# Performance work log

Measured on AMD Instinct MI355X. Metric: run time of the kernel, lower is better.

Reference implementation:

```python
import jax, jax.numpy as jnp
import numpy as np

N = 100_000
E = 1_000_000
F_IN = 128
F_OUT = 64
NHOP = 2


def _xavier(k, shape, gain=1.414):
    fan_in, fan_out = shape
    std = gain * np.sqrt(2.0 / (fan_in + fan_out))
    return (jax.random.normal(k, shape) * std).astype(jnp.float32)


def setup_inputs() -> dict:
    key = jax.random.key(0)
    ks = jax.random.split(key, 8)
    x = jax.random.normal(ks[0], (N, F_IN), jnp.float32)
    edge_index = jax.random.randint(ks[1], (2, E), 0, N)
    edge_attr = jax.random.uniform(ks[2], (E,), jnp.float32)
    W0 = _xavier(ks[3], (F_IN, F_OUT))
    W1 = _xavier(ks[4], (F_IN, F_OUT))
    b0 = jnp.zeros((F_OUT,), jnp.float32)
    b1 = jnp.zeros((F_OUT,), jnp.float32)
    fc0 = _xavier(ks[5], (F_OUT, 1))
    fc1 = _xavier(ks[6], (F_OUT, 1))
    bf0 = jnp.zeros((1,), jnp.float32)
    bf1 = jnp.zeros((1,), jnp.float32)
    return dict(x=x, edge_index=edge_index, edge_attr=edge_attr,
                W0=W0, b0=b0, W1=W1, b1=b1,
                fc0=fc0, bf0=bf0, fc1=fc1, bf1=bf1)


def _spmm(row, col, val, v, n):
    # (A v)[r] = sum over edges (r -> c) of val * v[c]
    return jax.ops.segment_sum(val[:, None] * v[col], row, num_segments=n)


def _adaptive_enc(y, fc, bf):
    # NodeAdaptiveEncoder (eval mode): relu(y) + sigmoid(y@fc+bf) * min(y, 0)
    g = jax.nn.sigmoid(y @ fc + bf)  # [N, 1]
    return jnp.where(y < 0, 0.0, y) + g * jnp.where(y > 0, 0.0, y)


def reference(x, edge_index, edge_attr, W0, b0, W1, b1, fc0, bf0, fc1, bf1):
    n = x.shape[0]
    row, col = edge_index[0], edge_index[1]
    ones = jnp.ones((n, 1), x.dtype)
    params = [(W0, b0, fc0, bf0), (W1, b1, fc1, bf1)]
    outs = []
    for hop in range(NHOP):
        W, b, fc, bf = params[hop]
        h = x @ W  # [N, F_OUT]
        # identity attention; row_uniform norm of A^(hop+1) factors as
        # (A^(hop+1) h) / (A^(hop+1) 1) -- exact since spspmm sums duplicates.
        agg, deg = h, ones
        for _ in range(hop + 1):
            agg = _spmm(row, col, edge_attr, agg, n)
            deg = _spmm(row, col, edge_attr, deg, n)
        safe_deg = jnp.where(deg > 0, deg, 1.0)
        y = jnp.where(deg > 0, agg / safe_deg, 0.0)  # NaN mask for empty rows
        y = y + b
        outs.append(_adaptive_enc(y, fc, bf))
    return jnp.concatenate(outs, axis=1)  # [N, NHOP * F_OUT]
```

## Files before the change

kernel.cpp:

```cpp
#include <hip/hip_runtime.h>

#define F_IN 128
#define F_ALL 128
#define F_HOP 64

#define RPB_BITS 9
#define RPB 512
#define KB_MAX 256
#define NBLK_BIN 256
#define BCAP 16

typedef unsigned int uint;
typedef unsigned short ushort;
typedef __attribute__((ext_vector_type(8))) short short8v;
typedef __attribute__((ext_vector_type(4))) float float4v;

__device__ __forceinline__ uint pack_bf16(float lo, float hi) {
    uint ul = __float_as_uint(lo), uh = __float_as_uint(hi);
    ul += 0x7FFFu + ((ul >> 16) & 1u);
    uh += 0x7FFFu + ((uh >> 16) & 1u);
    return (ul >> 16) | (uh & 0xFFFF0000u);
}
__device__ __forceinline__ float bf_lo(uint h) { return __uint_as_float(h << 16); }
__device__ __forceinline__ float bf_hi(uint h) { return __uint_as_float(h & 0xFFFF0000u); }
__device__ __forceinline__ ushort to_bf16(float x) {
    uint u = __float_as_uint(x);
    u += 0x7FFFu + ((u >> 16) & 1u);
    return (ushort)(u >> 16);
}

__global__ __launch_bounds__(256) void gemm_mfma_kernel(
    const float* __restrict__ x, const float* __restrict__ W0,
    const float* __restrict__ W1, uint* __restrict__ H2, int N) {
    __shared__ ushort Wlds[16384];

    {
        const int t = threadIdx.x;
        #pragma unroll
        for (int i = 0; i < 8; ++i) {
            const int e    = t + 256 * i;
            const int lane = e & 63;
            const int tile = e >> 6;
            const int kt   = tile >> 3;
            const int nt   = tile & 7;
            const int k0   = kt * 32 + (lane >> 4) * 8;
            const int n    = nt * 16 + (lane & 15);
            const float* src = (n < 64) ? (W0 + n) : (W1 + (n - 64));
            float v[8];
            #pragma unroll
            for (int j = 0; j < 8; ++j) v[j] = src[(size_t)(k0 + j) * F_HOP];
            uint4 o;
            o.x = pack_bf16(v[0], v[1]);
            o.y = pack_bf16(v[2], v[3]);
            o.z = pack_bf16(v[4], v[5]);
            o.w = pack_bf16(v[6], v[7]);
            *((uint4*)Wlds + e) = o;
        }
    }
    __syncthreads();

    const int wv   = threadIdx.x >> 6;
    const int lane = threadIdx.x & 63;
    const int rbase = blockIdx.x * 64 + wv * 16;
    if (rbase >= N) return;

    const int m    = lane & 15;
    const int quad = lane >> 4;
    const float* xrow = x + (size_t)(rbase + m) * F_IN + quad * 8;

    float4v acc[8];
    #pragma unroll
    for (int t = 0; t < 8; ++t) acc[t] = (float4v){0.f, 0.f, 0.f, 0.f};

    #pragma unroll
    for (int kt = 0; kt < 4; ++kt) {
        const float4 xa = *(const float4*)(xrow + kt * 32);
        const float4 xb = *(const float4*)(xrow + kt * 32 + 4);
        union { uint4 u; short8v s; } av;
        av.u.x = pack_bf16(xa.x, xa.y);
        av.u.y = pack_bf16(xa.z, xa.w);
        av.u.z = pack_bf16(xb.x, xb.y);
        av.u.w = pack_bf16(xb.z, xb.w);
        #pragma unroll
        for (int nt = 0; nt < 8; ++nt) {
            union { uint4 u; short8v s; } bv;
            bv.u = *((const uint4*)Wlds + (kt * 8 + nt) * 64 + lane);
            acc[nt] = __builtin_amdgcn_mfma_f32_16x16x32_bf16(av.s, bv.s, acc[nt], 0, 0, 0);
        }
    }

    #pragma unroll
    for (int t = 0; t < 4; ++t) {
        #pragma unroll
        for (int i = 0; i < 4; ++i) {
            const int r = rbase + quad * 4 + i;
            H2[(size_t)r * F_HOP + t * 16 + m] = pack_bf16(acc[t][i], acc[t + 4][i]);
        }
    }
}

__global__ __launch_bounds__(256) void bucket_hist_kernel(
    const int* __restrict__ ei, int* __restrict__ bhist, int E, int K) {
    __shared__ int h[KB_MAX];
    for (int i = threadIdx.x; i < K; i += 256) h[i] = 0;
    __syncthreads();
    const int chunk = (E + NBLK_BIN - 1) / NBLK_BIN;
    const int s = blockIdx.x * chunk;
    const int e = min(s + chunk, E);
    for (int j = s + threadIdx.x; j < e; j += 256)
        atomicAdd(&h[ei[j] >> RPB_BITS], 1);
    __syncthreads();
    for (int i = threadIdx.x; i < K; i += 256)
        bhist[blockIdx.x * KB_MAX + i] = h[i];
}

__global__ __launch_bounds__(256) void bucket_scan_kernel(
    int* __restrict__ bhist, int* __restrict__ bbase,
    int* __restrict__ rowptr, int E, int K, int N) {
    __shared__ int wsum[4];
    const int t = threadIdx.x;
    int s = 0;
    if (t < K)
        for (int i = 0; i < NBLK_BIN; ++i) s += bhist[i * KB_MAX + t];
    int v = s;
    #pragma unroll
    for (int d = 1; d < 64; d <<= 1) {
        int u = __shfl_up(v, (unsigned)d, 64);
        if ((t & 63) >= d) v += u;
    }
    if ((t & 63) == 63) wsum[t >> 6] = v;
    __syncthreads();
    int off = 0;
    #pragma unroll
    for (int i = 0; i < 4; ++i) if (i < (t >> 6)) off += wsum[i];
    const int excl = off + v - s;
    if (t < K) {
        bbase[t] = excl;
        int run = excl;
        for (int i = 0; i < NBLK_BIN; ++i) {
            const int idx = i * KB_MAX + t;
            const int c = bhist[idx];
            bhist[idx] = run;
            run += c;
        }
    }
    if (t == 0) { bbase[K] = E; rowptr[N] = E; }
}

__global__ __launch_bounds__(256) void bin_kernel(
    const int* __restrict__ ei, const float* __restrict__ ea,
    const int* __restrict__ bloc, int2* __restrict__ gbuf, int E, int K) {
    __shared__ int buf[KB_MAX * (2 * BCAP + 1)];
    __shared__ int lcnt[KB_MAX];
    __shared__ int cur[KB_MAX];
    for (int i = threadIdx.x; i < K; i += 256) {
        lcnt[i] = 0;
        cur[i] = bloc[blockIdx.x * KB_MAX + i];
    }
    __syncthreads();
    const int chunk = (E + NBLK_BIN - 1) / NBLK_BIN;
    const int s0 = blockIdx.x * chunk;
    const int e0 = min(s0 + chunk, E);
    for (int base = s0; base < e0; base += 256) {
        const int j = base + threadIdx.x;
        if (j < e0) {
            const int r = ei[j];
            const int c = ei[E + j];
            const int vv = __float_as_int(ea[j]);
            const int b = r >> RPB_BITS;
            const int w0 = c | ((r & (RPB - 1)) << 17);
            const int pos = atomicAdd(&lcnt[b], 1);
            if (pos < BCAP) {
                const int boff = b * (2 * BCAP + 1) + 2 * pos;
                buf[boff] = w0; buf[boff + 1] = vv;
            } else {
                const int gp = atomicAdd(&cur[b], 1);
                gbuf[gp] = make_int2(w0, vv);
            }
        }
        __syncthreads();
        for (int b = threadIdx.x; b < K; b += 256) {
            int c = lcnt[b]; if (c > BCAP) c = BCAP;
            if (c >= 8) {
                const int n = c & ~7;
                const int gp = cur[b]; cur[b] = gp + n;
                const int boff = b * (2 * BCAP + 1);
                for (int i = 0; i < n; ++i)
                    gbuf[gp + i] = make_int2(buf[boff + 2 * i], buf[boff + 2 * i + 1]);
                for (int i = n; i < c; ++i) {
                    buf[boff + 2 * (i - n)]     = buf[boff + 2 * i];
                    buf[boff + 2 * (i - n) + 1] = buf[boff + 2 * i + 1];
                }
                lcnt[b] = c - n;
            } else {
                lcnt[b] = c;
            }
        }
        __syncthreads();
    }
    for (int b = threadIdx.x; b < K; b += 256) {
        int c = lcnt[b]; if (c > BCAP) c = BCAP;
        if (c > 0) {
            const int gp = cur[b];
            const int boff = b * (2 * BCAP + 1);
            for (int i = 0; i < c; ++i)
                gbuf[gp + i] = make_int2(buf[boff + 2 * i], buf[boff + 2 * i + 1]);
        }
    }
}

__global__ __launch_bounds__(256) void sort_kernel(
    const int* __restrict__ bbase, const int2* __restrict__ gbuf,
    int2* __restrict__ ecv, int* __restrict__ rowptr, int N) {
    __shared__ int cnt[RPB];
    __shared__ int nxt[RPB];
    __shared__ int wsum[4];
    const int b = blockIdx.x;
    const int t = threadIdx.x;
    const int bstart = bbase[b], bend = bbase[b + 1];
    const int row0 = b << RPB_BITS;
    for (int i = t; i < RPB; i += 256) cnt[i] = 0;
    __syncthreads();
    for (int j = bstart + t; j < bend; j += 256)
        atomicAdd(&cnt[(gbuf[j].x >> 17) & (RPB - 1)], 1);
    __syncthreads();
    const int c0 = cnt[2 * t], c1 = cnt[2 * t + 1];
    const int s = c0 + c1;
    int v = s;
    #pragma unroll
    for (int d = 1; d < 64; d <<= 1) {
        int u = __shfl_up(v, (unsigned)d, 64);
        if ((t & 63) >= d) v += u;
    }
    if ((t & 63) == 63) wsum[t >> 6] = v;
    __syncthreads();
    int off = 0;
    #pragma unroll
    for (int i = 0; i < 4; ++i) if (i < (t >> 6)) off += wsum[i];
    const int e0 = off + v - s;
    nxt[2 * t]     = e0;
    nxt[2 * t + 1] = e0 + c0;
    const int r0 = row0 + 2 * t, r1 = row0 + 2 * t + 1;
    if (r0 < N) rowptr[r0] = bstart + e0;
    if (r1 < N) rowptr[r1] = bstart + e0 + c0;
    __syncthreads();
    for (int j = bstart + t; j < bend; j += 256) {
        const int2 p = gbuf[j];
        const int lr = (p.x >> 17) & (RPB - 1);
        const int pos = atomicAdd(&nxt[lr], 1);
        ecv[bstart + pos] = make_int2(p.x & 0x1FFFF, p.y);
    }
}

__global__ __launch_bounds__(256) void pass1_kernel(
    const int* __restrict__ rowptr, const int2* __restrict__ ecv,
    const uint* __restrict__ H2,
    const float* __restrict__ b0, const float* __restrict__ fc0,
    const float* __restrict__ bf0,
    float* __restrict__ out, ushort* __restrict__ T16,
    float* __restrict__ dg1, int N) {
    int r = blockIdx.x * 4 + (threadIdx.x >> 6);
    r = __builtin_amdgcn_readfirstlane(r);
    if (r >= N) return;
    const int f = threadIdx.x & 63;
    const int jb = rowptr[r], je = rowptr[r + 1];
    float s0a = 0.f, s0b = 0.f, s0c = 0.f, s0d = 0.f;
    float s1a = 0.f, s1b = 0.f, s1c = 0.f, s1d = 0.f;
    float da = 0.f, db = 0.f;
    int j = jb;
    for (; j + 4 <= je; j += 4) {
        const int2 e0 = ecv[j], e1 = ecv[j + 1], e2 = ecv[j + 2], e3 = ecv[j + 3];
        const uint h0 = H2[(size_t)e0.x * F_HOP + f];
        const uint h1 = H2[(size_t)e1.x * F_HOP + f];
        const uint h2 = H2[(size_t)e2.x * F_HOP + f];
        const uint h3 = H2[(size_t)e3.x * F_HOP + f];
        const float v0 = __int_as_float(e0.y), v1 = __int_as_float(e1.y);
        const float v2 = __int_as_float(e2.y), v3 = __int_as_float(e3.y);
        da += v0 + v1; db += v2 + v3;
        s0a = fmaf(v0, bf_lo(h0), s0a); s1a = fmaf(v0, bf_hi(h0), s1a);
        s0b = fmaf(v1, bf_lo(h1), s0b); s1b = fmaf(v1, bf_hi(h1), s1b);
        s0c = fmaf(v2, bf_lo(h2), s0c); s1c = fmaf(v2, bf_hi(h2), s1c);
        s0d = fmaf(v3, bf_lo(h3), s0d); s1d = fmaf(v3, bf_hi(h3), s1d);
    }
    for (; j < je; ++j) {
        const int2 e0 = ecv[j];
        const uint h0 = H2[(size_t)e0.x * F_HOP + f];
        const float v0 = __int_as_float(e0.y);
        da += v0;
        s0a = fmaf(v0, bf_lo(h0), s0a); s1a = fmaf(v0, bf_hi(h0), s1a);
    }
    const float acc0 = (s0a + s0b) + (s0c + s0d);
    const float acc1 = (s1a + s1b) + (s1c + s1d);
    const float d = (da + db);
    T16[(size_t)r * F_HOP + f] = to_bf16(acc1);
    if (f == 0) dg1[r] = d;
    float y = (d > 0.f ? acc0 / d : 0.f) + b0[f];
    float t = y * fc0[f];
    #pragma unroll
    for (int m = 1; m < 64; m <<= 1) t += __shfl_xor(t, m, 64);
    const float g = 1.f / (1.f + __expf(-(t + bf0[0])));
    out[(size_t)r * F_ALL + f] = fmaxf(y, 0.f) + g * fminf(y, 0.f);
}

__global__ __launch_bounds__(256) void pass2_kernel(
    const int* __restrict__ rowptr, const int2* __restrict__ ecv,
    const ushort* __restrict__ T16, const float* __restrict__ dg1,
    const float* __restrict__ b1, const float* __restrict__ fc1,
    const float* __restrict__ bf1,
    float* __restrict__ out, int N) {
    int r = blockIdx.x * 4 + (threadIdx.x >> 6);
    r = __builtin_amdgcn_readfirstlane(r);
    if (r >= N) return;
    const int f = threadIdx.x & 63;
    const int jb = rowptr[r], je = rowptr[r + 1];
    float sa = 0.f, sb = 0.f, sc = 0.f, sd = 0.f;
    float da = 0.f, db = 0.f;
    int j = jb;
    for (; j + 4 <= je; j += 4) {
        const int2 e0 = ecv[j], e1 = ecv[j + 1], e2 = ecv[j + 2], e3 = ecv[j + 3];
        const ushort t0 = T16[(size_t)e0.x * F_HOP + f];
        const ushort t1 = T16[(size_t)e1.x * F_HOP + f];
        const ushort t2 = T16[(size_t)e2.x * F_HOP + f];
        const ushort t3 = T16[(size_t)e3.x * F_HOP + f];
        const float g0 = dg1[e0.x], g1 = dg1[e1.x], g2 = dg1[e2.x], g3 = dg1[e3.x];
        const float v0 = __int_as_float(e0.y), v1 = __int_as_float(e1.y);
        const float v2 = __int_as_float(e2.y), v3 = __int_as_float(e3.y);
        da = fmaf(v0, g0, da); db = fmaf(v1, g1, db);
        da = fmaf(v2, g2, da); db = fmaf(v3, g3, db);
        sa = fmaf(v0, __uint_as_float((uint)t0 << 16), sa);
        sb = fmaf(v1, __uint_as_float((uint)t1 << 16), sb);
        sc = fmaf(v2, __uint_as_float((uint)t2 << 16), sc);
        sd = fmaf(v3, __uint_as_float((uint)t3 << 16), sd);
    }
    for (; j < je; ++j) {
        const int2 e0 = ecv[j];
        const ushort t0 = T16[(size_t)e0.x * F_HOP + f];
        const float v0 = __int_as_float(e0.y);
        da = fmaf(v0, dg1[e0.x], da);
        sa = fmaf(v0, __uint_as_float((uint)t0 << 16), sa);
    }
    const float acc = (sa + sb) + (sc + sd);
    const float d2 = da + db;
    float y = (d2 > 0.f ? acc / d2 : 0.f) + b1[f];
    float t = y * fc1[f];
    #pragma unroll
    for (int m = 1; m < 64; m <<= 1) t += __shfl_xor(t, m, 64);
    const float g = 1.f / (1.f + __expf(-(t + bf1[0])));
    out[(size_t)r * F_ALL + F_HOP + f] = fmaxf(y, 0.f) + g * fminf(y, 0.f);
}

extern "C" void kernel_launch(void* const* d_in, const int* in_sizes, int n_in,
                              void* d_out, int out_size, void* d_ws, size_t ws_size,
                              hipStream_t stream) {
    const float* x   = (const float*)d_in[0];
    const int*   ei  = (const int*)  d_in[1];
    const float* ea  = (const float*)d_in[2];
    const float* W0  = (const float*)d_in[3];
    const float* b0  = (const float*)d_in[4];
    const float* W1  = (const float*)d_in[5];
    const float* b1  = (const float*)d_in[6];
    const float* fc0 = (const float*)d_in[7];
    const float* bf0 = (const float*)d_in[8];
    const float* fc1 = (const float*)d_in[9];
    const float* bf1 = (const float*)d_in[10];
    float* out = (float*)d_out;

    const int N = in_sizes[0] / F_IN;
    const int E = in_sizes[2];
    const int K = (N + RPB - 1) >> RPB_BITS;

    uint*   H2   = (uint*)d_ws;
    ushort* T16  = (ushort*)(H2 + (size_t)N * F_HOP);
    float*  dg1  = (float*)(T16 + (size_t)N * F_HOP);
    int2*   gbuf = (int2*)(dg1 + (size_t)((N + 3) & ~3));
    int2*   ecv  = gbuf + (size_t)E;
    int*    bhist = (int*)(ecv + (size_t)E);
    int*    bbase = bhist + (size_t)NBLK_BIN * KB_MAX;
    int*    rowptr = bbase + (KB_MAX + 8);

    gemm_mfma_kernel<<<(N + 63) / 64, 256, 0, stream>>>(x, W0, W1, H2, N);

    bucket_hist_kernel<<<NBLK_BIN, 256, 0, stream>>>(ei, bhist, E, K);
    bucket_scan_kernel<<<1, 256, 0, stream>>>(bhist, bbase, rowptr, E, K, N);
    bin_kernel<<<NBLK_BIN, 256, 0, stream>>>(ei, ea, bhist, gbuf, E, K);
    sort_kernel<<<K, 256, 0, stream>>>(bbase, gbuf, ecv, rowptr, N);

    pass1_kernel<<<(N + 3) / 4, 256, 0, stream>>>(
        rowptr, ecv, H2, b0, fc0, bf0, out, T16, dg1, N);

    pass2_kernel<<<(N + 3) / 4, 256, 0, stream>>>(
        rowptr, ecv, T16, dg1, b1, fc1, bf1, out, N);
}
```

Measured before the change: 283.7 us.

## Process four rows per wavefront with vectorized 16-lane gathers in SpMM passes

Both aggregation passes now map 16 lanes to each row, so one wavefront handles four rows instead of one. Each lane loads 16-byte (pass1) or 8-byte (pass2) vectors covering four features rather than one dword or ushort. The gating reduction shrinks to a 16-lane shuffle and the outputs are written as float4. The goal is fewer, wider memory instructions per edge and fewer wave-level edge loops, at the cost of more divergence when rows in the same wave have different degrees.

```diff
diff --git a/kernel.cpp b/kernel.cpp
--- a/kernel.cpp
+++ b/kernel.cpp
@@ -259,47 +259,79 @@
     const float* __restrict__ bf0,
     float* __restrict__ out, ushort* __restrict__ T16,
     float* __restrict__ dg1, int N) {
-    int r = blockIdx.x * 4 + (threadIdx.x >> 6);
-    r = __builtin_amdgcn_readfirstlane(r);
+    const int lane = threadIdx.x & 63;
+    const int g    = lane >> 4;
+    const int l    = lane & 15;
+    const int r = blockIdx.x * 16 + (threadIdx.x >> 6) * 4 + g;
     if (r >= N) return;
-    const int f = threadIdx.x & 63;
+    const int f0 = l * 4;
+    const uint* __restrict__ H2b = H2 + f0;
     const int jb = rowptr[r], je = rowptr[r + 1];
-    float s0a = 0.f, s0b = 0.f, s0c = 0.f, s0d = 0.f;
-    float s1a = 0.f, s1b = 0.f, s1c = 0.f, s1d = 0.f;
-    float da = 0.f, db = 0.f;
+
+    float s00 = 0.f, s01 = 0.f, s02 = 0.f, s03 = 0.f;
+    float s10 = 0.f, s11 = 0.f, s12 = 0.f, s13 = 0.f;
+    float d = 0.f;
     int j = jb;
     for (; j + 4 <= je; j += 4) {
         const int2 e0 = ecv[j], e1 = ecv[j + 1], e2 = ecv[j + 2], e3 = ecv[j + 3];
-        const uint h0 = H2[(size_t)e0.x * F_HOP + f];
-        const uint h1 = H2[(size_t)e1.x * F_HOP + f];
-        const uint h2 = H2[(size_t)e2.x * F_HOP + f];
-        const uint h3 = H2[(size_t)e3.x * F_HOP + f];
+        const uint4 h0 = *(const uint4*)(H2b + (size_t)e0.x * F_HOP);
+        const uint4 h1 = *(const uint4*)(H2b + (size_t)e1.x * F_HOP);
+        const uint4 h2 = *(const uint4*)(H2b + (size_t)e2.x * F_HOP);
+        const uint4 h3 = *(const uint4*)(H2b + (size_t)e3.x * F_HOP);
         const float v0 = __int_as_float(e0.y), v1 = __int_as_float(e1.y);
         const float v2 = __int_as_float(e2.y), v3 = __int_as_float(e3.y);
-        da += v0 + v1; db += v2 + v3;
-        s0a = fmaf(v0, bf_lo(h0), s0a); s1a = fmaf(v0, bf_hi(h0), s1a);
-        s0b = fmaf(v1, bf_lo(h1), s0b); s1b = fmaf(v1, bf_hi(h1), s1b);
-        s0c = fmaf(v2, bf_lo(h2), s0c); s1c = fmaf(v2, bf_hi(h2), s1c);
-        s0d = fmaf(v3, bf_lo(h3), s0d); s1d = fmaf(v3, bf_hi(h3), s1d);
+        d += (v0 + v1) + (v2 + v3);
+        s00 = fmaf(v0, bf_lo(h0.x), s00); s10 = fmaf(v0, bf_hi(h0.x), s10);
+        s01 = fmaf(v0, bf_lo(h0.y), s01); s11 = fmaf(v0, bf_hi(h0.y), s11);
+        s02 = fmaf(v0, bf_lo(h0.z), s02); s12 = fmaf(v0, bf_hi(h0.z), s12);
+        s03 = fmaf(v0, bf_lo(h0.w), s03); s13 = fmaf(v0, bf_hi(h0.w), s13);
+        s00 = fmaf(v1, bf_lo(h1.x), s00); s10 = fmaf(v1, bf_hi(h1.x), s10);
+        s01 = fmaf(v1, bf_lo(h1.y), s01); s11 = fmaf(v1, bf_hi(h1.y), s11);
+        s02 = fmaf(v1, bf_lo(h1.z), s02); s12 = fmaf(v1, bf_hi(h1.z), s12);
+        s03 = fmaf(v1, bf_lo(h1.w), s03); s13 = fmaf(v1, bf_hi(h1.w), s13);
+        s00 = fmaf(v2, bf_lo(h2.x), s00); s10 = fmaf(v2, bf_hi(h2.x), s10);
+        s01 = fmaf(v2, bf_lo(h2.y), s01); s11 = fmaf(v2, bf_hi(h2.y), s11);
+        s02 = fmaf(v2, bf_lo(h2.z), s02); s12 = fmaf(v2, bf_hi(h2.z), s12);
+        s03 = fmaf(v2, bf_lo(h2.w), s03); s13 = fmaf(v2, bf_hi(h2.w), s13);
+        s00 = fmaf(v3, bf_lo(h3.x), s00); s10 = fmaf(v3, bf_hi(h3.x), s10);
+        s01 = fmaf(v3, bf_lo(h3.y), s01); s11 = fmaf(v3, bf_hi(h3.y), s11);
+        s02 = fmaf(v3, bf_lo(h3.z), s02); s12 = fmaf(v3, bf_hi(h3.z), s12);
+        s03 = fmaf(v3, bf_lo(h3.w), s03); s13 = fmaf(v3, bf_hi(h3.w), s13);
     }
     for (; j < je; ++j) {
         const int2 e0 = ecv[j];
-        const uint h0 = H2[(size_t)e0.x * F_HOP + f];
+        const uint4 h0 = *(const uint4*)(H2b + (size_t)e0.x * F_HOP);
         const float v0 = __int_as_float(e0.y);
-        da += v0;
-        s0a = fmaf(v0, bf_lo(h0), s0a); s1a = fmaf(v0, bf_hi(h0), s1a);
-    }
-    const float acc0 = (s0a + s0b) + (s0c + s0d);
-    const float acc1 = (s1a + s1b) + (s1c + s1d);
-    const float d = (da + db);
-    T16[(size_t)r * F_HOP + f] = to_bf16(acc1);
-    if (f == 0) dg1[r] = d;
-    float y = (d > 0.f ? acc0 / d : 0.f) + b0[f];
-    float t = y * fc0[f];
-    #pragma unroll
-    for (int m = 1; m < 64; m <<= 1) t += __shfl_xor(t, m, 64);
-    const float g = 1.f / (1.f + __expf(-(t + bf0[0])));
-    out[(size_t)r * F_ALL + f] = fmaxf(y, 0.f) + g * fminf(y, 0.f);
+        d += v0;
+        s00 = fmaf(v0, bf_lo(h0.x), s00); s10 = fmaf(v0, bf_hi(h0.x), s10);
+        s01 = fmaf(v0, bf_lo(h0.y), s01); s11 = fmaf(v0, bf_hi(h0.y), s11);
+        s02 = fmaf(v0, bf_lo(h0.z), s02); s12 = fmaf(v0, bf_hi(h0.z), s12);
+        s03 = fmaf(v0, bf_lo(h0.w), s03); s13 = fmaf(v0, bf_hi(h0.w), s13);
+    }
+
+    uint2 tw;
+    tw.x = pack_bf16(s10, s11);
+    tw.y = pack_bf16(s12, s13);
+    *(uint2*)(T16 + (size_t)r * F_HOP + f0) = tw;
+    if (l == 0) dg1[r] = d;
+
+    const float inv = (d > 0.f) ? 1.f / d : 0.f;
+    const float4 bb = *(const float4*)(b0 + f0);
+    const float4 ff = *(const float4*)(fc0 + f0);
+    const float y0 = s00 * inv + bb.x;
+    const float y1 = s01 * inv + bb.y;
+    const float y2 = s02 * inv + bb.z;
+    const float y3 = s03 * inv + bb.w;
+    float t = y0 * ff.x + y1 * ff.y + y2 * ff.z + y3 * ff.w;
+    #pragma unroll
+    for (int m = 1; m < 16; m <<= 1) t += __shfl_xor(t, m, 64);
+    const float gg = 1.f / (1.f + __expf(-(t + bf0[0])));
+    float4 o;
+    o.x = fmaxf(y0, 0.f) + gg * fminf(y0, 0.f);
+    o.y = fmaxf(y1, 0.f) + gg * fminf(y1, 0.f);
+    o.z = fmaxf(y2, 0.f) + gg * fminf(y2, 0.f);
+    o.w = fmaxf(y3, 0.f) + gg * fminf(y3, 0.f);
+    *(float4*)(out + (size_t)r * F_ALL + f0) = o;
 }
 
 __global__ __launch_bounds__(256) void pass2_kernel(
@@ -308,45 +340,64 @@
     const float* __restrict__ b1, const float* __restrict__ fc1,
     const float* __restrict__ bf1,
     float* __restrict__ out, int N) {
-    int r = blockIdx.x * 4 + (threadIdx.x >> 6);
-    r = __builtin_amdgcn_readfirstlane(r);
+    const int lane = threadIdx.x & 63;
+    const int g    = lane >> 4;
+    const int l    = lane & 15;
+    const int r = blockIdx.x * 16 + (threadIdx.x >> 6) * 4 + g;
     if (r >= N) return;
-    const int f = threadIdx.x & 63;
+    const int f0 = l * 4;
+    const ushort* __restrict__ Tb = T16 + f0;
     const int jb = rowptr[r], je = rowptr[r + 1];
-    float sa = 0.f, sb = 0.f, sc = 0.f, sd = 0.f;
-    float da = 0.f, db = 0.f;
+
+    float s0 = 0.f, s1 = 0.f, s2 = 0.f, s3 = 0.f;
+    float d2 = 0.f;
     int j = jb;
     for (; j + 4 <= je; j += 4) {
         const int2 e0 = ecv[j], e1 = ecv[j + 1], e2 = ecv[j + 2], e3 = ecv[j + 3];
-        const ushort t0 = T16[(size_t)e0.x * F_HOP + f];
-        const ushort t1 = T16[(size_t)e1.x * F_HOP + f];
-        const ushort t2 = T16[(size_t)e2.x * F_HOP + f];
-        const ushort t3 = T16[(size_t)e3.x * F_HOP + f];
+        const uint2 t0 = *(const uint2*)(Tb + (size_t)e0.x * F_HOP);
+        const uint2 t1 = *(const uint2*)(Tb + (size_t)e1.x * F_HOP);
+        const uint2 t2 = *(const uint2*)(Tb + (size_t)e2.x * F_HOP);
+        const uint2 t3 = *(const uint2*)(Tb + (size_t)e3.x * F_HOP);
         const float g0 = dg1[e0.x], g1 = dg1[e1.x], g2 = dg1[e2.x], g3 = dg1[e3.x];
         const float v0 = __int_as_float(e0.y), v1 = __int_as_float(e1.y);
         const float v2 = __int_as_float(e2.y), v3 = __int_as_float(e3.y);
-        da = fmaf(v0, g0, da); db = fmaf(v1, g1, db);
-        da = fmaf(v2, g2, da); db = fmaf(v3, g3, db);
-        sa = fmaf(v0, __uint_as_float((uint)t0 << 16), sa);
-        sb = fmaf(v1, __uint_as_float((uint)t1 << 16), sb);
-        sc = fmaf(v2, __uint_as_float((uint)t2 << 16), sc);
-        sd = fmaf(v3, __uint_as_float((uint)t3 << 16), sd);
+        d2 = fmaf(v0, g0, d2); d2 = fmaf(v1, g1, d2);
+        d2 = fmaf(v2, g2, d2); d2 = fmaf(v3, g3, d2);
+        s0 = fmaf(v0, bf_lo(t0.x), s0); s1 = fmaf(v0, bf_hi(t0.x), s1);
+        s2 = fmaf(v0, bf_lo(t0.y), s2); s3 = fmaf(v0, bf_hi(t0.y), s3);
+        s0 = fmaf(v1, bf_lo(t1.x), s0); s1 = fmaf(v1, bf_hi(t1.x), s1);
+        s2 = fmaf(v1, bf_lo(t1.y), s2); s3 = fmaf(v1, bf_hi(t1.y), s3);
+        s0 = fmaf(v2, bf_lo(t2.x), s0); s1 = fmaf(v2, bf_hi(t2.x), s1);
+        s2 = fmaf(v2, bf_lo(t2.y), s2); s3 = fmaf(v2, bf_hi(t2.y), s3);
+        s0 = fmaf(v3, bf_lo(t3.x), s0); s1 = fmaf(v3, bf_hi(t3.x), s1);
+        s2 = fmaf(v3, bf_lo(t3.y), s2); s3 = fmaf(v3, bf_hi(t3.y), s3);
     }
     for (; j < je; ++j) {
         const int2 e0 = ecv[j];
-        const ushort t0 = T16[(size_t)e0.x * F_HOP + f];
+        const uint2 t0 = *(const uint2*)(Tb + (size_t)e0.x * F_HOP);
         const float v0 = __int_as_float(e0.y);
-        da = fmaf(v0, dg1[e0.x], da);
-        sa = fmaf(v0, __uint_as_float((uint)t0 << 16), sa);
-    }
-    const float acc = (sa + sb) + (sc + sd);
-    const float d2 = da + db;
-    float y = (d2 > 0.f ? acc / d2 : 0.f) + b1[f];
-    float t = y * fc1[f];
-    #pragma unroll
-    for (int m = 1; m < 64; m <<= 1) t += __shfl_xor(t, m, 64);
-    const float g = 1.f / (1.f + __expf(-(t + bf1[0])));
-    out[(size_t)r * F_ALL + F_HOP + f] = fmaxf(y, 0.f) + g * fminf(y, 0.f);
+        d2 = fmaf(v0, dg1[e0.x], d2);
+        s0 = fmaf(v0, bf_lo(t0.x), s0); s1 = fmaf(v0, bf_hi(t0.x), s1);
+        s2 = fmaf(v0, bf_lo(t0.y), s2); s3 = fmaf(v0, bf_hi(t0.y), s3);
+    }
+
+    const float inv = (d2 > 0.f) ? 1.f / d2 : 0.f;
+    const float4 bb = *(const float4*)(b1 + f0);
+    const float4 ff = *(const float4*)(fc1 + f0);
+    const float y0 = s0 * inv + bb.x;
+    const float y1 = s1 * inv + bb.y;
+    const float y2 = s2 * inv + bb.z;
+    const float y3 = s3 * inv + bb.w;
+    float t = y0 * ff.x + y1 * ff.y + y2 * ff.z + y3 * ff.w;
+    #pragma unroll
+    for (int m = 1; m < 16; m <<= 1) t += __shfl_xor(t, m, 64);
+    const float gg = 1.f / (1.f + __expf(-(t + bf1[0])));
+    float4 o;
+    o.x = fmaxf(y0, 0.f) + gg * fminf(y0, 0.f);
+    o.y = fmaxf(y1, 0.f) + gg * fminf(y1, 0.f);
+    o.z = fmaxf(y2, 0.f) + gg * fminf(y2, 0.f);
+    o.w = fmaxf(y3, 0.f) + gg * fminf(y3, 0.f);
+    *(float4*)(out + (size_t)r * F_ALL + F_HOP + f0) = o;
 }
 
 extern "C" void kernel_launch(void* const* d_in, const int* in_sizes, int n_in,
@@ -385,9 +436,9 @@
     bin_kernel<<<NBLK_BIN, 256, 0, stream>>>(ei, ea, bhist, gbuf, E, K);
     sort_kernel<<<K, 256, 0, stream>>>(bbase, gbuf, ecv, rowptr, N);
 
-    pass1_kernel<<<(N + 3) / 4, 256, 0, stream>>>(
+    pass1_kernel<<<(N + 15) / 16, 256, 0, stream>>>(
         rowptr, ecv, H2, b0, fc0, bf0, out, T16, dg1, N);
 
-    pass2_kernel<<<(N + 3) / 4, 256, 0, stream>>>(
+    pass2_kernel<<<(N + 15) / 16, 256, 0, stream>>>(
         rowptr, ecv, T16, dg1, b1, fc1, bf1, out, N);
 }
```

Result: faster. 258.3 us (-8.9%).
